# Kernel tuning notes

Hardware: AMD Instinct MI355X
Metric: run time of the kernel (lower is better)

The kernel has to match this reference:

```python
import jax, jax.numpy as jnp
import numpy as np

N = 100000          # nodes
E = 1600000         # edges (before self-loops)
F_IN = 256          # num_node_features
F_MID = F_IN // 2   # conv1 out = 128
HID = 128           # hidden_channels
OUT = 64            # num_label_features
G = 128             # num graphs in batch
NEG_SLOPE = 0.2


def setup_inputs() -> dict:
    key = jax.random.key(0)
    ks = jax.random.split(key, 16)
    s = 0.05
    return {
        "x": jax.random.normal(ks[0], (N, F_IN), dtype=jnp.float32),
        "edge_index": jax.random.randint(ks[1], (2, E), 0, N, dtype=jnp.int64),
        "batch": jnp.sort(jax.random.randint(ks[2], (N,), 0, G, dtype=jnp.int64)),
        # GATConv 1 (heads=1)
        "W1": jax.random.normal(ks[3], (F_IN, F_MID), jnp.float32) * s,
        "a1_src": jax.random.normal(ks[4], (F_MID,), jnp.float32) * s,
        "a1_dst": jax.random.normal(ks[5], (F_MID,), jnp.float32) * s,
        "b1": jnp.zeros((F_MID,), jnp.float32),
        # GATConv 2
        "W2": jax.random.normal(ks[6], (F_MID, HID), jnp.float32) * s,
        "a2_src": jax.random.normal(ks[7], (HID,), jnp.float32) * s,
        "a2_dst": jax.random.normal(ks[8], (HID,), jnp.float32) * s,
        "b2": jnp.zeros((HID,), jnp.float32),
        # GlobalAttention gate nn
        "gate_W": jax.random.normal(ks[9], (HID, 1), jnp.float32) * s,
        "gate_b": jnp.zeros((1,), jnp.float32),
        # final linear
        "lin_W": jax.random.normal(ks[10], (HID, OUT), jnp.float32) * s,
        "lin_b": jnp.zeros((OUT,), jnp.float32),
    }


def _gat_conv(x, edge_index, W, a_src, a_dst, bias):
    """PyG GATConv, heads=1, add_self_loops=True, negative_slope=0.2."""
    n = x.shape[0]
    h = x @ W                                   # [N, F]
    loop = jnp.arange(n, dtype=edge_index.dtype)
    src = jnp.concatenate([edge_index[0], loop])  # message sources j
    dst = jnp.concatenate([edge_index[1], loop])  # aggregation targets i
    # per-node attention logits, gathered per-edge
    al = (h @ a_src)[src] + (h @ a_dst)[dst]    # [E+N]
    al = jax.nn.leaky_relu(al, NEG_SLOPE)
    # segment softmax over incoming edges of each dst node
    m = jax.ops.segment_max(al, dst, num_segments=n)
    e = jnp.exp(al - m[dst])
    s = jax.ops.segment_sum(e, dst, num_segments=n)
    coef = e / (s[dst] + 1e-16)
    out = jax.ops.segment_sum(h[src] * coef[:, None], dst, num_segments=n)
    return out + bias


def reference(x, edge_index, batch, W1, a1_src, a1_dst, b1,
              W2, a2_src, a2_dst, b2, gate_W, gate_b, lin_W, lin_b):
    h = _gat_conv(x, edge_index, W1, a1_src, a1_dst, b1)
    h = jax.nn.relu(h)
    h = _gat_conv(h, edge_index, W2, a2_src, a2_dst, b2)
    # GlobalAttention pooling: segment softmax of gate over batch ids
    gate = (h @ gate_W + gate_b)[:, 0]          # [N]
    gm = jax.ops.segment_max(gate, batch, num_segments=G)
    ge = jnp.exp(gate - gm[batch])
    gs = jax.ops.segment_sum(ge, batch, num_segments=G)
    attn = ge / (gs[batch] + 1e-16)
    pooled = jax.ops.segment_sum(h * attn[:, None], batch, num_segments=G)  # [G, HID]
    pooled = jax.nn.relu(pooled)
    # dropout p=0.5 is identity at inference
    return pooled @ lin_W + lin_b               # [G, OUT]
```

## Files before the change

### kernel.cpp

```cpp
#include <hip/hip_runtime.h>
#include <hip/hip_bf16.h>
#include <math.h>

#define NNODES 100000
#define NEDGES 1600000
#define EN     1700000
#define F_IN   256
#define F_MID  128
#define HID    128
#define NG     128
#define NOUT   64
#define SCAN_CHUNK 2048
#define NCHUNK ((NNODES + SCAN_CHUNK - 1) / SCAN_CHUNK)
#define CHUNK  8

typedef unsigned int  u32;
typedef unsigned short u16;

__device__ __forceinline__ float bfl(u32 u) { return __uint_as_float(u << 16); }
__device__ __forceinline__ float bfh(u32 u) { return __uint_as_float(u & 0xFFFF0000u); }
__device__ __forceinline__ u32 f2bf(float f) {
    u32 x = __float_as_uint(f);
    return (x + 0x7FFFu + ((x >> 16) & 1u)) >> 16;
}

__device__ __forceinline__ void gload_lds4(const u32* g, u32* ldsbase) {
    __builtin_amdgcn_global_load_lds(
        (const __attribute__((address_space(1))) u32*)(uintptr_t)g,
        (__attribute__((address_space(3))) u32*)(u32)(uintptr_t)ldsbase,
        4, 0, 0);
}

__global__ __launch_bounds__(256) void k_init(int* deg, float* gs, float* pooled) {
    int i = blockIdx.x * 256 + threadIdx.x;
    if (i < NNODES) deg[i] = 1;
    if (i < NG) gs[i] = 0.f;
    if (i < NG * HID) pooled[i] = 0.f;
}

__global__ __launch_bounds__(256) void k_count(const int* __restrict__ ei, int* deg) {
    int e = blockIdx.x * 256 + threadIdx.x;
    if (e >= NEDGES) return;
    atomicAdd(&deg[ei[NEDGES + e]], 1);
}

__global__ __launch_bounds__(256) void k_scan_chunk(const int* __restrict__ deg,
                                                    int* rowptr, int* part) {
    __shared__ int sums[256];
    int c = blockIdx.x, t = threadIdx.x;
    int base = c * SCAN_CHUNK;
    int v[8]; int s = 0;
#pragma unroll
    for (int i = 0; i < 8; i++) {
        int idx = base + t * 8 + i;
        v[i] = (idx < NNODES) ? deg[idx] : 0;
        s += v[i];
    }
    sums[t] = s;
    __syncthreads();
    for (int off = 1; off < 256; off <<= 1) {
        int x = (t >= off) ? sums[t - off] : 0;
        __syncthreads();
        sums[t] += x;
        __syncthreads();
    }
    int run = (t == 0) ? 0 : sums[t - 1];
#pragma unroll
    for (int i = 0; i < 8; i++) {
        int idx = base + t * 8 + i;
        if (idx < NNODES) rowptr[idx] = run;
        run += v[i];
    }
    if (t == 255) part[c] = sums[255];
}

__global__ void k_scan_part(int* part, int nc) {
    if (threadIdx.x == 0) {
        int run = 0;
        for (int c = 0; c < nc; c++) { int v = part[c]; part[c] = run; run += v; }
    }
}

__global__ __launch_bounds__(256) void k_scan_add(int* rowptr, int* cursor,
                                                  const int* __restrict__ part) {
    int i = blockIdx.x * 256 + threadIdx.x;
    if (i >= NNODES) return;
    int v = rowptr[i] + part[i >> 11];
    rowptr[i] = v;
    cursor[i] = v;
}

__global__ __launch_bounds__(256) void k_fill(const int* __restrict__ ei,
                                              int* cursor, int2* meta0) {
    int e = blockIdx.x * 256 + threadIdx.x;
    if (e >= EN) return;
    int src, dst;
    if (e < NEDGES) { src = ei[e]; dst = ei[NEDGES + e]; }
    else            { src = dst = e - NEDGES; }
    int pos = atomicAdd(&cursor[dst], 1);
    meta0[pos] = make_int2(src, dst);
}

__global__ __launch_bounds__(256) void k_coef(const int2* __restrict__ meta0,
                                              const float* __restrict__ as_,
                                              const float* __restrict__ ad_,
                                              int2* __restrict__ meta1) {
    int e = blockIdx.x * 256 + threadIdx.x;
    if (e >= EN) return;
    int2 sd = meta0[e];
    float al = as_[sd.x] + ad_[sd.y];
    al = (al > 0.f) ? al : 0.2f * al;
    meta1[e] = make_int2(sd.x, __float_as_int(__expf(al)));
}

template <int K, bool ABF>
__global__ __launch_bounds__(256) void k_gemm(const void* __restrict__ Av,
                                              const float* __restrict__ B,
                                              u16* __restrict__ C, int M) {
    __shared__ float As[16][128];
    __shared__ float Bs[16][128];
    int bm = blockIdx.x * 128;
    int tid = threadIdx.x;
    int tx = tid & 15, ty = tid >> 4;
    float acc[8][8] = {};
    for (int k0 = 0; k0 < K; k0 += 16) {
#pragma unroll
        for (int q = tid; q < 512; q += 256) {
            int m = q >> 2, kq = (q & 3) << 2;
            int row = bm + m;
            if (ABF) {
                const u16* A = (const u16*)Av;
                uint2 v = make_uint2(0u, 0u);
                if (row < M) v = *(const uint2*)(A + (size_t)row * K + k0 + kq);
                As[kq + 0][m] = bfl(v.x); As[kq + 1][m] = bfh(v.x);
                As[kq + 2][m] = bfl(v.y); As[kq + 3][m] = bfh(v.y);
            } else {
                const float* A = (const float*)Av;
                float4 v = make_float4(0.f, 0.f, 0.f, 0.f);
                if (row < M) v = *(const float4*)(A + (size_t)row * K + k0 + kq);
                As[kq + 0][m] = v.x; As[kq + 1][m] = v.y;
                As[kq + 2][m] = v.z; As[kq + 3][m] = v.w;
            }
        }
#pragma unroll
        for (int q = tid; q < 512; q += 256) {
            int kk = q >> 5, n4 = (q & 31) << 2;
            *(float4*)(&Bs[kk][n4]) = *(const float4*)(B + (size_t)(k0 + kk) * 128 + n4);
        }
        __syncthreads();
#pragma unroll
        for (int kk = 0; kk < 16; kk++) {
            float a[8], b[8];
            *(float4*)(a)     = *(float4*)(&As[kk][ty * 8]);
            *(float4*)(a + 4) = *(float4*)(&As[kk][ty * 8 + 4]);
            *(float4*)(b)     = *(float4*)(&Bs[kk][tx * 8]);
            *(float4*)(b + 4) = *(float4*)(&Bs[kk][tx * 8 + 4]);
#pragma unroll
            for (int i = 0; i < 8; i++)
#pragma unroll
                for (int j = 0; j < 8; j++)
                    acc[i][j] = fmaf(a[i], b[j], acc[i][j]);
        }
        __syncthreads();
    }
#pragma unroll
    for (int i = 0; i < 8; i++) {
        int row = bm + ty * 8 + i;
        if (row < M) {
            uint4 o;
            o.x = f2bf(acc[i][0]) | (f2bf(acc[i][1]) << 16);
            o.y = f2bf(acc[i][2]) | (f2bf(acc[i][3]) << 16);
            o.z = f2bf(acc[i][4]) | (f2bf(acc[i][5]) << 16);
            o.w = f2bf(acc[i][6]) | (f2bf(acc[i][7]) << 16);
            *(uint4*)(C + (size_t)row * 128 + tx * 8) = o;
        }
    }
}

__global__ __launch_bounds__(256) void k_dots(const u32* __restrict__ h,
                                              const float* __restrict__ asrc,
                                              const float* __restrict__ adst,
                                              float* as_, float* ad_) {
    int wid = (blockIdx.x * 256 + threadIdx.x) >> 6;
    int lane = threadIdx.x & 63;
    if (wid >= NNODES) return;
    u32 u = h[(size_t)wid * 64 + lane];
    float vx = bfl(u), vy = bfh(u);
    float2 as2 = ((const float2*)asrc)[lane];
    float2 ad2 = ((const float2*)adst)[lane];
    float s = vx * as2.x + vy * as2.y;
    float d = vx * ad2.x + vy * ad2.y;
#pragma unroll
    for (int off = 32; off; off >>= 1) {
        s += __shfl_xor(s, off);
        d += __shfl_xor(d, off);
    }
    if (lane == 0) { as_[wid] = s; ad_[wid] = d; }
}

template <bool RELU, bool GATE, bool OUTBF>
__global__ __launch_bounds__(256) void k_agg(
    const u32* __restrict__ h, const int2* __restrict__ meta,
    const int* __restrict__ rowptr, const int* __restrict__ rowend,
    const float* __restrict__ bias, void* __restrict__ outv,
    const float* __restrict__ gateW, const float* __restrict__ gateB,
    float* __restrict__ gatev, float* __restrict__ gs,
    const int* __restrict__ batch) {
    __shared__ u32 lbuf[4][CHUNK * 64];
    int tid = threadIdx.x;
    int w = tid >> 6, lane = tid & 63;
    int wid = blockIdx.x * 4 + w;
    if (wid >= NNODES) return;
    int row = rowptr[wid];
    int dg = rowend[wid] - row;
    const int2* mp = meta + row;
    u32* wb = &lbuf[w][0];

    float ssum = 0.f, ax = 0.f, ay = 0.f;
    for (int cb = 0; cb < dg; cb += CHUNK) {
        asm volatile("s_waitcnt lgkmcnt(0)" ::: "memory");
        int2 mm[CHUNK];
#pragma unroll
        for (int j = 0; j < CHUNK; j++) {
            int idx = cb + j;
            mm[j] = mp[(idx < dg) ? idx : dg - 1];
        }
#pragma unroll
        for (int j = 0; j < CHUNK; j++)
            gload_lds4(h + (size_t)mm[j].x * 64 + lane, wb + j * 64);
        asm volatile("s_waitcnt vmcnt(0)" ::: "memory");
#pragma unroll
        for (int j = 0; j < CHUNK; j++) {
            float ev = ((cb + j) < dg) ? __int_as_float(mm[j].y) : 0.f;
            u32 u = wb[j * 64 + lane];
            ssum += ev;
            ax = fmaf(ev, bfl(u), ax);
            ay = fmaf(ev, bfh(u), ay);
        }
    }

    float inv = 1.f / (ssum + 1e-16f);
    float2 b2v = ((const float2*)bias)[lane];
    float o0 = ax * inv + b2v.x;
    float o1 = ay * inv + b2v.y;
    if (RELU) { o0 = fmaxf(o0, 0.f); o1 = fmaxf(o1, 0.f); }
    if (OUTBF) {
        ((u32*)outv)[(size_t)wid * 64 + lane] = f2bf(o0) | (f2bf(o1) << 16);
    } else {
        ((float2*)((float*)outv + (size_t)wid * 128))[lane] = make_float2(o0, o1);
    }
    if (GATE) {
        float2 gw = ((const float2*)gateW)[lane];
        float g = o0 * gw.x + o1 * gw.y;
#pragma unroll
        for (int off = 32; off; off >>= 1) g += __shfl_xor(g, off);
        if (lane == 0) {
            float ge = __expf(g + gateB[0]);
            gatev[wid] = ge;
            atomicAdd(&gs[batch[wid]], ge);
        }
    }
}

__global__ __launch_bounds__(128) void k_pool(const float* __restrict__ h,
                                              const float* __restrict__ gatev,
                                              const float* __restrict__ gs,
                                              const int* __restrict__ batch,
                                              float* pooled) {
    int t = threadIdx.x;
    int chunk = (NNODES + gridDim.x - 1) / gridDim.x;
    int s0 = blockIdx.x * chunk;
    int s1 = s0 + chunk; if (s1 > NNODES) s1 = NNODES;
    if (s0 >= s1) return;
    int curg = batch[s0];
    float invs = 1.f / (gs[curg] + 1e-16f);
    float acc = 0.f;
    for (int i = s0; i < s1; i++) {
        int g = batch[i];
        if (g != curg) {
            atomicAdd(&pooled[curg * 128 + t], acc);
            acc = 0.f; curg = g;
            invs = 1.f / (gs[g] + 1e-16f);
        }
        acc += h[(size_t)i * 128 + t] * (gatev[i] * invs);
    }
    atomicAdd(&pooled[curg * 128 + t], acc);
}

__global__ __launch_bounds__(64) void k_final(const float* __restrict__ pooled,
                                              const float* __restrict__ linW,
                                              const float* __restrict__ linb,
                                              float* __restrict__ out) {
    __shared__ float rowv[128];
    int g = blockIdx.x, t = threadIdx.x;
    rowv[t]      = fmaxf(pooled[g * 128 + t], 0.f);
    rowv[t + 64] = fmaxf(pooled[g * 128 + 64 + t], 0.f);
    __syncthreads();
    float acc = linb[t];
#pragma unroll 8
    for (int k = 0; k < 128; k++) acc = fmaf(rowv[k], linW[k * 64 + t], acc);
    out[g * 64 + t] = acc;
}

extern "C" void kernel_launch(void* const* d_in, const int* in_sizes, int n_in,
                              void* d_out, int out_size, void* d_ws, size_t ws_size,
                              hipStream_t stream) {
    const float* x     = (const float*)d_in[0];
    const int*   ei    = (const int*)d_in[1];
    const int*   batch = (const int*)d_in[2];
    const float* W1    = (const float*)d_in[3];
    const float* a1s   = (const float*)d_in[4];
    const float* a1d   = (const float*)d_in[5];
    const float* b1    = (const float*)d_in[6];
    const float* W2    = (const float*)d_in[7];
    const float* a2s   = (const float*)d_in[8];
    const float* a2d   = (const float*)d_in[9];
    const float* b2    = (const float*)d_in[10];
    const float* gateW = (const float*)d_in[11];
    const float* gateB = (const float*)d_in[12];
    const float* linW  = (const float*)d_in[13];
    const float* linb  = (const float*)d_in[14];
    float* out = (float*)d_out;

    char* p = (char*)d_ws;
    auto alloc = [&](size_t bytes) -> void* {
        void* r = (void*)p;
        p += (bytes + 255) & ~(size_t)255;
        return r;
    };
    u16*   hb     = (u16*)alloc((size_t)NNODES * 128 * 2);
    char*  region = (char*)alloc((size_t)NNODES * 128 * 4);
    u16*   h1a    = (u16*)region;
    int2*  meta0  = (int2*)(region + (size_t)NNODES * 128 * 2);
    float* bufF   = (float*)region;
    int2*  meta1  = (int2*)alloc((size_t)EN * 8);
    float* as_    = (float*)alloc((size_t)NNODES * 4);
    float* ad_    = (float*)alloc((size_t)NNODES * 4);
    float* gatev  = (float*)alloc((size_t)NNODES * 4);
    int*   deg    = (int*)alloc((size_t)NNODES * 4);
    int*   rowptr = (int*)alloc((size_t)NNODES * 4);
    int*   cursor = (int*)alloc((size_t)NNODES * 4);
    int*   part   = (int*)alloc(64 * 4);
    float* gs     = (float*)alloc(NG * 4);
    float* pooled = (float*)alloc((size_t)NG * HID * 4);

    const int gN   = (NNODES + 255) / 256;
    const int gE   = (NEDGES + 255) / 256;
    const int gEN  = (EN + 255) / 256;
    const int gW   = (NNODES + 3) / 4;

    k_init<<<gN, 256, 0, stream>>>(deg, gs, pooled);
    k_count<<<gE, 256, 0, stream>>>(ei, deg);
    k_scan_chunk<<<NCHUNK, 256, 0, stream>>>(deg, rowptr, part);
    k_scan_part<<<1, 64, 0, stream>>>(part, NCHUNK);
    k_scan_add<<<gN, 256, 0, stream>>>(rowptr, cursor, part);
    k_fill<<<gEN, 256, 0, stream>>>(ei, cursor, meta0);

    k_gemm<256, false><<<(NNODES + 127) / 128, 256, 0, stream>>>(x, W1, hb, NNODES);
    k_dots<<<gW, 256, 0, stream>>>((const u32*)hb, a1s, a1d, as_, ad_);
    k_coef<<<gEN, 256, 0, stream>>>(meta0, as_, ad_, meta1);
    k_agg<true, false, true><<<gW, 256, 0, stream>>>((const u32*)hb, meta1,
                                                     rowptr, cursor, b1, h1a,
                                                     nullptr, nullptr, nullptr,
                                                     nullptr, nullptr);
    k_gemm<128, true><<<(NNODES + 127) / 128, 256, 0, stream>>>(h1a, W2, hb, NNODES);
    k_dots<<<gW, 256, 0, stream>>>((const u32*)hb, a2s, a2d, as_, ad_);
    k_coef<<<gEN, 256, 0, stream>>>(meta0, as_, ad_, meta1);
    k_agg<false, true, false><<<gW, 256, 0, stream>>>((const u32*)hb, meta1,
                                                      rowptr, cursor, b2, bufF,
                                                      gateW, gateB, gatev, gs, batch);
    k_pool<<<512, 128, 0, stream>>>(bufF, gatev, gs, batch, pooled);
    k_final<<<NG, 64, 0, stream>>>(pooled, linW, linb, out);
}
```

Baseline: 1.217 ms.

## Pad CSR rows to multiples of eight and gather rows with 16-byte loads

Each node's row in the CSR is padded up to a multiple of eight edges. The padding slots hold zero coefficients, so the aggregation loop needs no bounds checks and can read sources and coefficients as aligned int4/float4 vectors. Edge metadata moves from interleaved int2 to separate src, dst and coefficient arrays. Aggregation drops the LDS global_load_lds staging: each quarter-wave gathers a whole 256-byte neighbour row with uint4 loads, and the four partial sums are combined with cross-lane shuffles. This adds an init kernel and extra padded storage, and the split buffers no longer alias the feature region, so the workspace grows.

```diff
diff --git a/kernel.cpp b/kernel.cpp
--- a/kernel.cpp
+++ b/kernel.cpp
@@ -5,6 +5,7 @@
 #define NNODES 100000
 #define NEDGES 1600000
 #define EN     1700000
+#define ALLOCE (EN + 7 * NNODES + 64)
 #define F_IN   256
 #define F_MID  128
 #define HID    128
@@ -12,7 +13,6 @@
 #define NOUT   64
 #define SCAN_CHUNK 2048
 #define NCHUNK ((NNODES + SCAN_CHUNK - 1) / SCAN_CHUNK)
-#define CHUNK  8
 
 typedef unsigned int  u32;
 typedef unsigned short u16;
@@ -24,18 +24,18 @@
     return (x + 0x7FFFu + ((x >> 16) & 1u)) >> 16;
 }
 
-__device__ __forceinline__ void gload_lds4(const u32* g, u32* ldsbase) {
-    __builtin_amdgcn_global_load_lds(
-        (const __attribute__((address_space(1))) u32*)(uintptr_t)g,
-        (__attribute__((address_space(3))) u32*)(u32)(uintptr_t)ldsbase,
-        4, 0, 0);
-}
-
 __global__ __launch_bounds__(256) void k_init(int* deg, float* gs, float* pooled) {
     int i = blockIdx.x * 256 + threadIdx.x;
     if (i < NNODES) deg[i] = 1;
     if (i < NG) gs[i] = 0.f;
     if (i < NG * HID) pooled[i] = 0.f;
+}
+
+__global__ __launch_bounds__(256) void k_meta_init(int* srcs, int* dsts) {
+    int i = blockIdx.x * 256 + threadIdx.x;
+    if (i >= ALLOCE) return;
+    srcs[i] = 0;
+    dsts[i] = -1;
 }
 
 __global__ __launch_bounds__(256) void k_count(const int* __restrict__ ei, int* deg) {
@@ -53,7 +53,7 @@
 #pragma unroll
     for (int i = 0; i < 8; i++) {
         int idx = base + t * 8 + i;
-        v[i] = (idx < NNODES) ? deg[idx] : 0;
+        v[i] = (idx < NNODES) ? ((deg[idx] + 7) & ~7) : 0;
         s += v[i];
     }
     sums[t] = s;
@@ -91,26 +91,32 @@
 }
 
 __global__ __launch_bounds__(256) void k_fill(const int* __restrict__ ei,
-                                              int* cursor, int2* meta0) {
+                                              int* cursor, int* srcs, int* dsts) {
     int e = blockIdx.x * 256 + threadIdx.x;
     if (e >= EN) return;
     int src, dst;
     if (e < NEDGES) { src = ei[e]; dst = ei[NEDGES + e]; }
     else            { src = dst = e - NEDGES; }
     int pos = atomicAdd(&cursor[dst], 1);
-    meta0[pos] = make_int2(src, dst);
-}
-
-__global__ __launch_bounds__(256) void k_coef(const int2* __restrict__ meta0,
+    srcs[pos] = src;
+    dsts[pos] = dst;
+}
+
+__global__ __launch_bounds__(256) void k_coef(const int* __restrict__ srcs,
+                                              const int* __restrict__ dsts,
                                               const float* __restrict__ as_,
                                               const float* __restrict__ ad_,
-                                              int2* __restrict__ meta1) {
+                                              float* __restrict__ evs) {
     int e = blockIdx.x * 256 + threadIdx.x;
-    if (e >= EN) return;
-    int2 sd = meta0[e];
-    float al = as_[sd.x] + ad_[sd.y];
-    al = (al > 0.f) ? al : 0.2f * al;
-    meta1[e] = make_int2(sd.x, __float_as_int(__expf(al)));
+    if (e >= ALLOCE) return;
+    int d = dsts[e];
+    float ev = 0.f;
+    if (d >= 0) {
+        float al = as_[srcs[e]] + ad_[d];
+        al = (al > 0.f) ? al : 0.2f * al;
+        ev = __expf(al);
+    }
+    evs[e] = ev;
 }
 
 template <int K, bool ABF>
@@ -200,60 +206,98 @@
 
 template <bool RELU, bool GATE, bool OUTBF>
 __global__ __launch_bounds__(256) void k_agg(
-    const u32* __restrict__ h, const int2* __restrict__ meta,
-    const int* __restrict__ rowptr, const int* __restrict__ rowend,
+    const u32* __restrict__ h, const int* __restrict__ srcs,
+    const float* __restrict__ evs, const int* __restrict__ rowptr,
+    const int* __restrict__ rowend,
     const float* __restrict__ bias, void* __restrict__ outv,
     const float* __restrict__ gateW, const float* __restrict__ gateB,
     float* __restrict__ gatev, float* __restrict__ gs,
     const int* __restrict__ batch) {
-    __shared__ u32 lbuf[4][CHUNK * 64];
     int tid = threadIdx.x;
     int w = tid >> 6, lane = tid & 63;
     int wid = blockIdx.x * 4 + w;
     if (wid >= NNODES) return;
     int row = rowptr[wid];
     int dg = rowend[wid] - row;
-    const int2* mp = meta + row;
-    u32* wb = &lbuf[w][0];
-
-    float ssum = 0.f, ax = 0.f, ay = 0.f;
-    for (int cb = 0; cb < dg; cb += CHUNK) {
-        asm volatile("s_waitcnt lgkmcnt(0)" ::: "memory");
-        int2 mm[CHUNK];
-#pragma unroll
-        for (int j = 0; j < CHUNK; j++) {
-            int idx = cb + j;
-            mm[j] = mp[(idx < dg) ? idx : dg - 1];
-        }
-#pragma unroll
-        for (int j = 0; j < CHUNK; j++)
-            gload_lds4(h + (size_t)mm[j].x * 64 + lane, wb + j * 64);
-        asm volatile("s_waitcnt vmcnt(0)" ::: "memory");
-#pragma unroll
-        for (int j = 0; j < CHUNK; j++) {
-            float ev = ((cb + j) < dg) ? __int_as_float(mm[j].y) : 0.f;
-            u32 u = wb[j * 64 + lane];
-            ssum += ev;
-            ax = fmaf(ev, bfl(u), ax);
-            ay = fmaf(ev, bfh(u), ay);
-        }
-    }
+    int q = lane >> 4;
+    int i = lane & 15;
+
+    float ssum = 0.f;
+    float2 a0 = {0.f, 0.f}, a1 = {0.f, 0.f}, a2 = {0.f, 0.f}, a3 = {0.f, 0.f};
+
+#pragma unroll 2
+    for (int cb = 0; cb < dg; cb += 8) {
+        int4   s03 = *(const int4*)(srcs + row + cb);
+        int4   s47 = *(const int4*)(srcs + row + cb + 4);
+        float4 e03 = *(const float4*)(evs + row + cb);
+        float4 e47 = *(const float4*)(evs + row + cb + 4);
+        int   tA0 = (q & 1) ? s03.y : s03.x;
+        int   tA1 = (q & 1) ? s03.w : s03.z;
+        int   sA  = (q & 2) ? tA1 : tA0;
+        float fA0 = (q & 1) ? e03.y : e03.x;
+        float fA1 = (q & 1) ? e03.w : e03.z;
+        float eA  = (q & 2) ? fA1 : fA0;
+        int   tB0 = (q & 1) ? s47.y : s47.x;
+        int   tB1 = (q & 1) ? s47.w : s47.z;
+        int   sB  = (q & 2) ? tB1 : tB0;
+        float fB0 = (q & 1) ? e47.y : e47.x;
+        float fB1 = (q & 1) ? e47.w : e47.z;
+        float eB  = (q & 2) ? fB1 : fB0;
+        uint4 vA = *(const uint4*)(h + (size_t)sA * 64 + 4 * i);
+        uint4 vB = *(const uint4*)(h + (size_t)sB * 64 + 4 * i);
+        ssum += eA + eB;
+        a0.x = fmaf(eA, bfl(vA.x), a0.x); a0.y = fmaf(eA, bfh(vA.x), a0.y);
+        a1.x = fmaf(eA, bfl(vA.y), a1.x); a1.y = fmaf(eA, bfh(vA.y), a1.y);
+        a2.x = fmaf(eA, bfl(vA.z), a2.x); a2.y = fmaf(eA, bfh(vA.z), a2.y);
+        a3.x = fmaf(eA, bfl(vA.w), a3.x); a3.y = fmaf(eA, bfh(vA.w), a3.y);
+        a0.x = fmaf(eB, bfl(vB.x), a0.x); a0.y = fmaf(eB, bfh(vB.x), a0.y);
+        a1.x = fmaf(eB, bfl(vB.y), a1.x); a1.y = fmaf(eB, bfh(vB.y), a1.y);
+        a2.x = fmaf(eB, bfl(vB.z), a2.x); a2.y = fmaf(eB, bfh(vB.z), a2.y);
+        a3.x = fmaf(eB, bfl(vB.w), a3.x); a3.y = fmaf(eB, bfh(vB.w), a3.y);
+    }
+    ssum += __shfl_xor(ssum, 16);  ssum += __shfl_xor(ssum, 32);
+    a0.x += __shfl_xor(a0.x, 16);  a0.x += __shfl_xor(a0.x, 32);
+    a0.y += __shfl_xor(a0.y, 16);  a0.y += __shfl_xor(a0.y, 32);
+    a1.x += __shfl_xor(a1.x, 16);  a1.x += __shfl_xor(a1.x, 32);
+    a1.y += __shfl_xor(a1.y, 16);  a1.y += __shfl_xor(a1.y, 32);
+    a2.x += __shfl_xor(a2.x, 16);  a2.x += __shfl_xor(a2.x, 32);
+    a2.y += __shfl_xor(a2.y, 16);  a2.y += __shfl_xor(a2.y, 32);
+    a3.x += __shfl_xor(a3.x, 16);  a3.x += __shfl_xor(a3.x, 32);
+    a3.y += __shfl_xor(a3.y, 16);  a3.y += __shfl_xor(a3.y, 32);
 
     float inv = 1.f / (ssum + 1e-16f);
-    float2 b2v = ((const float2*)bias)[lane];
-    float o0 = ax * inv + b2v.x;
-    float o1 = ay * inv + b2v.y;
-    if (RELU) { o0 = fmaxf(o0, 0.f); o1 = fmaxf(o1, 0.f); }
-    if (OUTBF) {
-        ((u32*)outv)[(size_t)wid * 64 + lane] = f2bf(o0) | (f2bf(o1) << 16);
-    } else {
-        ((float2*)((float*)outv + (size_t)wid * 128))[lane] = make_float2(o0, o1);
+    float4 bA = ((const float4*)bias)[2 * i];
+    float4 bB = ((const float4*)bias)[2 * i + 1];
+    float f0 = a0.x * inv + bA.x, f1 = a0.y * inv + bA.y;
+    float f2 = a1.x * inv + bA.z, f3 = a1.y * inv + bA.w;
+    float f4 = a2.x * inv + bB.x, f5 = a2.y * inv + bB.y;
+    float f6 = a3.x * inv + bB.z, f7 = a3.y * inv + bB.w;
+    if (RELU) {
+        f0 = fmaxf(f0, 0.f); f1 = fmaxf(f1, 0.f); f2 = fmaxf(f2, 0.f);
+        f3 = fmaxf(f3, 0.f); f4 = fmaxf(f4, 0.f); f5 = fmaxf(f5, 0.f);
+        f6 = fmaxf(f6, 0.f); f7 = fmaxf(f7, 0.f);
+    }
+    if (lane < 16) {
+        if (OUTBF) {
+            uint4 o;
+            o.x = f2bf(f0) | (f2bf(f1) << 16);
+            o.y = f2bf(f2) | (f2bf(f3) << 16);
+            o.z = f2bf(f4) | (f2bf(f5) << 16);
+            o.w = f2bf(f6) | (f2bf(f7) << 16);
+            ((uint4*)outv)[(size_t)wid * 16 + i] = o;
+        } else {
+            float* o = (float*)outv + (size_t)wid * 128 + 8 * i;
+            ((float4*)o)[0] = make_float4(f0, f1, f2, f3);
+            ((float4*)o)[1] = make_float4(f4, f5, f6, f7);
+        }
     }
     if (GATE) {
-        float2 gw = ((const float2*)gateW)[lane];
-        float g = o0 * gw.x + o1 * gw.y;
-#pragma unroll
-        for (int off = 32; off; off >>= 1) g += __shfl_xor(g, off);
+        float4 gA = ((const float4*)gateW)[2 * i];
+        float4 gB = ((const float4*)gateW)[2 * i + 1];
+        float g = f0 * gA.x + f1 * gA.y + f2 * gA.z + f3 * gA.w
+                + f4 * gB.x + f5 * gB.y + f6 * gB.z + f7 * gB.w;
+#pragma unroll
+        for (int off = 8; off; off >>= 1) g += __shfl_xor(g, off);
         if (lane == 0) {
             float ge = __expf(g + gateB[0]);
             gatev[wid] = ge;
@@ -329,11 +373,11 @@
         return r;
     };
     u16*   hb     = (u16*)alloc((size_t)NNODES * 128 * 2);
-    char*  region = (char*)alloc((size_t)NNODES * 128 * 4);
-    u16*   h1a    = (u16*)region;
-    int2*  meta0  = (int2*)(region + (size_t)NNODES * 128 * 2);
-    float* bufF   = (float*)region;
-    int2*  meta1  = (int2*)alloc((size_t)EN * 8);
+    u16*   h1a    = (u16*)alloc((size_t)NNODES * 128 * 2);
+    float* bufF   = (float*)alloc((size_t)NNODES * 128 * 4);
+    int*   srcs   = (int*)alloc((size_t)ALLOCE * 4);
+    int*   dsts   = (int*)alloc((size_t)ALLOCE * 4);
+    float* evs    = (float*)alloc((size_t)ALLOCE * 4);
     float* as_    = (float*)alloc((size_t)NNODES * 4);
     float* ad_    = (float*)alloc((size_t)NNODES * 4);
     float* gatev  = (float*)alloc((size_t)NNODES * 4);
@@ -347,6 +391,7 @@
     const int gN   = (NNODES + 255) / 256;
     const int gE   = (NEDGES + 255) / 256;
     const int gEN  = (EN + 255) / 256;
+    const int gAE  = (ALLOCE + 255) / 256;
     const int gW   = (NNODES + 3) / 4;
 
     k_init<<<gN, 256, 0, stream>>>(deg, gs, pooled);
@@ -354,19 +399,20 @@
     k_scan_chunk<<<NCHUNK, 256, 0, stream>>>(deg, rowptr, part);
     k_scan_part<<<1, 64, 0, stream>>>(part, NCHUNK);
     k_scan_add<<<gN, 256, 0, stream>>>(rowptr, cursor, part);
-    k_fill<<<gEN, 256, 0, stream>>>(ei, cursor, meta0);
+    k_meta_init<<<gAE, 256, 0, stream>>>(srcs, dsts);
+    k_fill<<<gEN, 256, 0, stream>>>(ei, cursor, srcs, dsts);
 
     k_gemm<256, false><<<(NNODES + 127) / 128, 256, 0, stream>>>(x, W1, hb, NNODES);
     k_dots<<<gW, 256, 0, stream>>>((const u32*)hb, a1s, a1d, as_, ad_);
-    k_coef<<<gEN, 256, 0, stream>>>(meta0, as_, ad_, meta1);
-    k_agg<true, false, true><<<gW, 256, 0, stream>>>((const u32*)hb, meta1,
+    k_coef<<<gAE, 256, 0, stream>>>(srcs, dsts, as_, ad_, evs);
+    k_agg<true, false, true><<<gW, 256, 0, stream>>>((const u32*)hb, srcs, evs,
                                                      rowptr, cursor, b1, h1a,
                                                      nullptr, nullptr, nullptr,
                                                      nullptr, nullptr);
     k_gemm<128, true><<<(NNODES + 127) / 128, 256, 0, stream>>>(h1a, W2, hb, NNODES);
     k_dots<<<gW, 256, 0, stream>>>((const u32*)hb, a2s, a2d, as_, ad_);
-    k_coef<<<gEN, 256, 0, stream>>>(meta0, as_, ad_, meta1);
-    k_agg<false, true, false><<<gW, 256, 0, stream>>>((const u32*)hb, meta1,
+    k_coef<<<gAE, 256, 0, stream>>>(srcs, dsts, as_, ad_, evs);
+    k_agg<false, true, false><<<gW, 256, 0, stream>>>((const u32*)hb, srcs, evs,
                                                       rowptr, cursor, b2, bufF,
                                                       gateW, gateB, gatev, gs, batch);
     k_pool<<<512, 128, 0, stream>>>(bufF, gatev, gs, batch, pooled);
```

New measurement: 1.242 ms (median of 2 runs). 2.1% more time.
